# Optimization experiments

Measured on AMD Instinct MI355X. Metric: run time of the kernel, lower is better.

Reference implementation:

```python
import jax, jax.numpy as jnp
import numpy as np

N = 100000      # nodes
F_IN = 256      # num_node_features
E = 1600000     # edges (before self-loops)
DIMS = [F_IN, 128, 100, 32, 2]  # GCNConv layer widths


def _glorot(key, fan_in, fan_out):
    s = jnp.sqrt(6.0 / (fan_in + fan_out))
    return jax.random.uniform(key, (fan_in, fan_out), jnp.float32, -s, s)


def setup_inputs() -> dict:
    key = jax.random.key(0)
    ks = jax.random.split(key, 10)
    x = jax.random.normal(ks[0], (N, F_IN), jnp.float32)
    edge_index = jax.random.randint(ks[1], (2, E), 0, N, jnp.int32)
    inp = {"x": x, "edge_index": edge_index}
    for i in range(4):
        inp[f"W{i+1}"] = _glorot(ks[2 + 2 * i], DIMS[i], DIMS[i + 1])
        inp[f"b{i+1}"] = jnp.zeros((DIMS[i + 1],), jnp.float32)
    return inp


def reference(x, edge_index, W1, b1, W2, b2, W3, b3, W4, b4):
    n = x.shape[0]
    loops = jnp.arange(n, dtype=edge_index.dtype)
    src = jnp.concatenate([edge_index[0], loops])  # [E+N]
    dst = jnp.concatenate([edge_index[1], loops])
    # symmetric normalization: deg^-1/2[src] * deg^-1/2[dst] (self-loops included)
    deg = jax.ops.segment_sum(jnp.ones_like(src, x.dtype), dst, num_segments=n)
    dis = jax.lax.rsqrt(jnp.maximum(deg, 1.0))
    norm = (dis[src] * dis[dst])[:, None]  # [E+N, 1]

    def conv(h, W, b):
        h = h @ W                                      # [N, out]
        msg = h[src] * norm                            # gather + scale [E+N, out]
        return jax.ops.segment_sum(msg, dst, num_segments=n) + b

    h = jax.nn.leaky_relu(conv(x, W1, b1), negative_slope=0.1)
    h = jax.nn.leaky_relu(conv(h, W2, b2), negative_slope=0.1)
    h = jax.nn.leaky_relu(conv(h, W3, b3), negative_slope=0.1)
    h = conv(h, W4, b4)
    return jax.nn.softmax(h, axis=-1)
```

## Files before the change

### kernel.cpp

```cpp
#include <hip/hip_runtime.h>
#include <math.h>


typedef unsigned short ushort_t;
typedef unsigned int   uint_t;
typedef short  bf16x8 __attribute__((ext_vector_type(8)));
typedef float  f32x4  __attribute__((ext_vector_type(4)));

#define BKT_SHIFT 8
#define BKT_CAP   5120
#define BIN_CHUNK 4096

__device__ __forceinline__ ushort_t f2bf(float f) {
    union { float f; uint_t u; } v; v.f = f;
    uint_t u = v.u;
    u += 0x7fffu + ((u >> 16) & 1u);
    return (ushort_t)(u >> 16);
}
__device__ __forceinline__ float bflo(uint_t u) {
    union { uint_t q; float f; } v; v.q = u << 16; return v.f;
}
__device__ __forceinline__ float bfhi(uint_t u) {
    union { uint_t q; float f; } v; v.q = u & 0xffff0000u; return v.f;
}


__global__ __launch_bounds__(256) void bin_kernel(const int* __restrict__ srcArr,
                                                  const int* __restrict__ dstArr,
                                                  int* __restrict__ bkt_cursor,
                                                  uint2* __restrict__ staging,
                                                  int E, int nb) {
    __shared__ int hist[512];
    __shared__ int base[512];
    for (int b = threadIdx.x; b < 512; b += 256) hist[b] = 0;
    __syncthreads();
    const int e0 = blockIdx.x * BIN_CHUNK;
    #pragma unroll 4
    for (int k = 0; k < BIN_CHUNK / 256; ++k) {
        int e = e0 + k * 256 + threadIdx.x;
        if (e < E) atomicAdd(&hist[dstArr[e] >> BKT_SHIFT], 1);
    }
    __syncthreads();
    for (int b = threadIdx.x; b < nb; b += 256) {
        int h = hist[b];
        base[b] = h ? atomicAdd(&bkt_cursor[b], h) : 0;
    }
    __syncthreads();
    for (int b = threadIdx.x; b < 512; b += 256) hist[b] = 0;
    __syncthreads();
    #pragma unroll 4
    for (int k = 0; k < BIN_CHUNK / 256; ++k) {
        int e = e0 + k * 256 + threadIdx.x;
        if (e < E) {
            int s = srcArr[e], d = dstArr[e];
            int b = d >> BKT_SHIFT;
            int p = atomicAdd(&hist[b], 1);
            int idx = base[b] + p;
            if (idx < BKT_CAP)
                staging[(size_t)b * BKT_CAP + idx] = make_uint2((uint_t)s, (uint_t)d);
        }
    }
}

__global__ __launch_bounds__(512) void bucket_scan_kernel(const int* __restrict__ bkt_cursor,
                                                          int* __restrict__ bkt_base,
                                                          int* __restrict__ row_start,
                                                          int nbkt, int n) {
    __shared__ int buf[512];
    int v = ((int)threadIdx.x < nbkt) ? min(bkt_cursor[threadIdx.x], BKT_CAP) : 0;
    buf[threadIdx.x] = v;
    __syncthreads();
    for (int off = 1; off < 512; off <<= 1) {
        int t = (threadIdx.x >= (unsigned)off) ? buf[threadIdx.x - off] : 0;
        __syncthreads();
        buf[threadIdx.x] += t;
        __syncthreads();
    }
    if ((int)threadIdx.x < nbkt) bkt_base[threadIdx.x] = buf[threadIdx.x] - v;
    if ((int)threadIdx.x == nbkt - 1) row_start[n] = buf[threadIdx.x];
}

__global__ __launch_bounds__(256) void csr_build2_kernel(const uint2* __restrict__ staging,
                                                         const int* __restrict__ bkt_cursor,
                                                         const int* __restrict__ bkt_base,
                                                         int* __restrict__ row_start,
                                                         float* __restrict__ dis,
                                                         int* __restrict__ csr_src, int n) {
    __shared__ int cnt[256];
    __shared__ int buf[256];
    __shared__ int rsS[256];
    __shared__ int seg[BKT_CAP];
    const int t  = threadIdx.x;
    const int b  = blockIdx.x;
    const int lo = b << BKT_SHIFT;
    const int nl = min(256, n - lo);
    cnt[t] = 0;
    __syncthreads();
    const int cntE = min(bkt_cursor[b], BKT_CAP);
    for (int e = t; e < cntE; e += 256) {
        uint2 p = staging[(size_t)b * BKT_CAP + e];
        atomicAdd(&cnt[(int)p.y - lo], 1);
    }
    __syncthreads();
    const int v = cnt[t];
    buf[t] = v;
    __syncthreads();
    for (int off = 1; off < 256; off <<= 1) {
        int tt = (t >= off) ? buf[t - off] : 0;
        __syncthreads();
        buf[t] += tt;
        __syncthreads();
    }
    rsS[t] = buf[t] - v;
    const int sbase = bkt_base[b];
    if (t < nl) {
        row_start[lo + t] = sbase + (buf[t] - v);
        dis[lo + t] = rsqrtf((float)(v + 1));
    }
    cnt[t] = 0;
    __syncthreads();
    for (int e = t; e < cntE; e += 256) {
        uint2 p = staging[(size_t)b * BKT_CAP + e];
        int ln = (int)p.y - lo;
        int q  = atomicAdd(&cnt[ln], 1);
        seg[rsS[ln] + q] = (int)p.x;
    }
    __syncthreads();
    for (int i = t; i < cntE; i += 256) csr_src[sbase + i] = seg[i];
}


__global__ void cast_bf16_kernel(const float* __restrict__ in, ushort_t* __restrict__ out, int n8) {
    int i = blockIdx.x * blockDim.x + threadIdx.x;
    if (i >= n8) return;
    const float4 f0 = ((const float4*)in)[2 * i];
    const float4 f1 = ((const float4*)in)[2 * i + 1];
    uint4 o;
    o.x = (uint_t)f2bf(f0.x) | ((uint_t)f2bf(f0.y) << 16);
    o.y = (uint_t)f2bf(f0.z) | ((uint_t)f2bf(f0.w) << 16);
    o.z = (uint_t)f2bf(f1.x) | ((uint_t)f2bf(f1.y) << 16);
    o.w = (uint_t)f2bf(f1.z) | ((uint_t)f2bf(f1.w) << 16);
    ((uint4*)out)[i] = o;
}

__global__ void wt_all_kernel(const float* __restrict__ W1, const float* __restrict__ W2,
                              const float* __restrict__ W3,
                              ushort_t* __restrict__ Wt1, ushort_t* __restrict__ Wt2,
                              ushort_t* __restrict__ Wt3) {
    int idx = blockIdx.x * blockDim.x + threadIdx.x;
    if (idx < 32768) {
        int nn = idx >> 8, k = idx & 255;
        Wt1[idx] = f2bf(W1[(size_t)k * 128 + nn]);
    } else if (idx < 49152) {
        int j = idx - 32768;
        int nn = j >> 7, k = j & 127;
        float v = (nn < 100) ? W2[(size_t)k * 100 + nn] : 0.f;
        Wt2[j] = f2bf(v);
    } else if (idx < 57344) {
        int j = idx - 49152;
        int nn = j >> 7, k = j & 127;
        float v = (k < 100 && nn < 32) ? W3[(size_t)k * 32 + nn] : 0.f;
        Wt3[j] = f2bf(v);
    }
}

template <int NFR>
__global__ __launch_bounds__(256) void gemm_tile(const ushort_t* __restrict__ A,
                                                 const ushort_t* __restrict__ Bt,
                                                 ushort_t* __restrict__ C,
                                                 const float* __restrict__ dis,
                                                 int M, int K, int lda, int ldb, int ldc) {
    constexpr int BN = NFR * 32;
    __shared__ __attribute__((aligned(16))) ushort_t As[64][72];
    __shared__ __attribute__((aligned(16))) ushort_t Bs[BN][72];

    const int t    = threadIdx.x;
    const int lane = t & 63;
    const int w    = t >> 6;
    const int wm   = w >> 1, wn = w & 1;
    const int m0   = blockIdx.x * 64;
    const int rsel = lane & 15;
    const int q    = lane >> 4;

    f32x4 acc[2][NFR];
    #pragma unroll
    for (int mi = 0; mi < 2; ++mi)
        #pragma unroll
        for (int ni = 0; ni < NFR; ++ni) acc[mi][ni] = (f32x4){0.f, 0.f, 0.f, 0.f};

    const int srow = t >> 3;
    const int scol = (t & 7) * 8;

    for (int k0 = 0; k0 < K; k0 += 64) {
        #pragma unroll
        for (int it = 0; it < 2; ++it) {
            int r = srow + it * 32;
            int gm = m0 + r;
            bf16x8 v = {0, 0, 0, 0, 0, 0, 0, 0};
            if (gm < M) v = *(const bf16x8*)(A + (size_t)gm * lda + k0 + scol);
            *(bf16x8*)&As[r][scol] = v;
        }
        #pragma unroll
        for (int it = 0; it < BN / 32; ++it) {
            int r = srow + it * 32;
            bf16x8 v = *(const bf16x8*)(Bt + (size_t)r * ldb + k0 + scol);
            *(bf16x8*)&Bs[r][scol] = v;
        }
        __syncthreads();
        #pragma unroll
        for (int ks = 0; ks < 2; ++ks) {
            const int kc = ks * 32 + q * 8;
            bf16x8 af[2], bfr[NFR];
            #pragma unroll
            for (int mi = 0; mi < 2; ++mi)
                af[mi] = *(const bf16x8*)&As[wm * 32 + mi * 16 + rsel][kc];
            #pragma unroll
            for (int ni = 0; ni < NFR; ++ni)
                bfr[ni] = *(const bf16x8*)&Bs[wn * (BN / 2) + ni * 16 + rsel][kc];
            #pragma unroll
            for (int mi = 0; mi < 2; ++mi)
                #pragma unroll
                for (int ni = 0; ni < NFR; ++ni)
                    acc[mi][ni] = __builtin_amdgcn_mfma_f32_16x16x32_bf16(
                        bfr[ni], af[mi], acc[mi][ni], 0, 0, 0);
        }
        __syncthreads();
    }

    #pragma unroll
    for (int mi = 0; mi < 2; ++mi) {
        const int gm = m0 + wm * 32 + mi * 16 + rsel;
        if (gm >= M) continue;
        const float d = dis[gm];
        #pragma unroll
        for (int ni = 0; ni < NFR; ++ni) {
            uint2 o;
            o.x = (uint_t)f2bf(acc[mi][ni][0] * d) | ((uint_t)f2bf(acc[mi][ni][1] * d) << 16);
            o.y = (uint_t)f2bf(acc[mi][ni][2] * d) | ((uint_t)f2bf(acc[mi][ni][3] * d) << 16);
            *(uint2*)(C + (size_t)gm * ldc + wn * (BN / 2) + ni * 16 + q * 4) = o;
        }
    }
}

template <int F>
__global__ void aggregate128_kernel(const ushort_t* __restrict__ h, const int* __restrict__ row_start,
                                    const int* __restrict__ csr_src,
                                    const float* __restrict__ dis, const float* __restrict__ bias,
                                    ushort_t* __restrict__ out, int n) {
    int wid  = threadIdx.x >> 6;
    int lane = threadIdx.x & 63;
    int node = blockIdx.x * 4 + wid;
    if (node >= n) return;
    const int q    = lane >> 4;
    const uint_t fbb = (uint_t)(lane & 15) << 4;
    const char* hb = (const char*)h;
    float a[8];
    #pragma unroll
    for (int j = 0; j < 8; ++j) a[j] = 0.f;

    int i = row_start[node], end = row_start[node + 1];

#define LOADR(S) (*(const uint4*)(hb + (((uint_t)(S) << 8) + fbb)))
#define ACC8(U)                                                     \
    do {                                                            \
        a[0] += bflo((U).x); a[1] += bfhi((U).x);                   \
        a[2] += bflo((U).y); a[3] += bfhi((U).y);                   \
        a[4] += bflo((U).z); a[5] += bfhi((U).z);                   \
        a[6] += bflo((U).w); a[7] += bfhi((U).w);                   \
    } while (0)

    #pragma unroll 2
    for (; i + 8 <= end; i += 8) {
        int sA = csr_src[i + q];
        int sB = csr_src[i + 4 + q];
        uint4 u = LOADR(sA);
        uint4 v = LOADR(sB);
        ACC8(u);
        ACC8(v);
    }
    int r = end - i;
    if (r > 0) {
        if (q < r) {
            uint4 u = LOADR(csr_src[i + q]);
            ACC8(u);
        }
        if (q + 4 < r) {
            uint4 v = LOADR(csr_src[i + 4 + q]);
            ACC8(v);
        }
    }

    #pragma unroll
    for (int j = 0; j < 8; ++j) {
        a[j] += __shfl_xor(a[j], 16);
        a[j] += __shfl_xor(a[j], 32);
    }

    if (q == 0) {
        uint4 su = LOADR(node);
        ACC8(su);
        float dn = dis[node];
        const int fb = (lane & 15) * 8;
        #pragma unroll
        for (int j = 0; j < 8; ++j) {
            float b = (fb + j < F) ? bias[fb + j] : 0.f;
            float v = a[j] * dn + b;
            v = (v > 0.f) ? v : 0.1f * v;
            if (fb + j >= F) v = 0.f;
            a[j] = v;
        }
        uint4 o;
        o.x = (uint_t)f2bf(a[0]) | ((uint_t)f2bf(a[1]) << 16);
        o.y = (uint_t)f2bf(a[2]) | ((uint_t)f2bf(a[3]) << 16);
        o.z = (uint_t)f2bf(a[4]) | ((uint_t)f2bf(a[5]) << 16);
        o.w = (uint_t)f2bf(a[6]) | ((uint_t)f2bf(a[7]) << 16);
        *(uint4*)((char*)out + (((uint_t)node << 8) + fbb)) = o;
    }
#undef ACC8
#undef LOADR
}

__global__ void aggregate32_kernel(const ushort_t* __restrict__ h, const int* __restrict__ row_start,
                                   const int* __restrict__ csr_src,
                                   const float* __restrict__ dis, const float* __restrict__ bias,
                                   ushort_t* __restrict__ out, int n) {
    int lane16 = threadIdx.x & 15;
    int node = blockIdx.x * (blockDim.x >> 4) + (threadIdx.x >> 4);
    if (node >= n) return;
    const uint_t fbb = (uint_t)lane16 << 2;
    const char* hb = (const char*)h;
#define LOADR32(S) (*(const uint_t*)(hb + (((uint_t)(S) << 6) + fbb)))
    uint_t v = LOADR32(node);
    float acc0 = bflo(v);
    float acc1 = bfhi(v);
    int i = row_start[node], end = row_start[node + 1];
    for (; i + 4 <= end; i += 4) {
        uint_t u0 = LOADR32(csr_src[i]);
        uint_t u1 = LOADR32(csr_src[i + 1]);
        uint_t u2 = LOADR32(csr_src[i + 2]);
        uint_t u3 = LOADR32(csr_src[i + 3]);
        acc0 += bflo(u0) + bflo(u1) + bflo(u2) + bflo(u3);
        acc1 += bfhi(u0) + bfhi(u1) + bfhi(u2) + bfhi(u3);
    }
    for (; i < end; ++i) {
        uint_t u = LOADR32(csr_src[i]);
        acc0 += bflo(u); acc1 += bfhi(u);
    }
#undef LOADR32
    float dn = dis[node];
    const int f0 = 2 * lane16;
    acc0 = acc0 * dn + bias[f0];
    acc1 = acc1 * dn + bias[f0 + 1];
    acc0 = (acc0 > 0.f) ? acc0 : 0.1f * acc0;
    acc1 = (acc1 > 0.f) ? acc1 : 0.1f * acc1;
    uint_t o = (uint_t)f2bf(acc0) | ((uint_t)f2bf(acc1) << 16);
    *(uint_t*)((char*)out + (((uint_t)node << 6) + fbb)) = o;
}

__global__ void gemm32x2_kernel(const ushort_t* __restrict__ H, const float* __restrict__ W4,
                                const float* __restrict__ dis, float* __restrict__ C, int n) {
    int node = blockIdx.x * blockDim.x + threadIdx.x;
    if (node >= n) return;
    const uint_t* row = (const uint_t*)(H + (size_t)node * 32);
    float a0 = 0.f, a1 = 0.f;
    #pragma unroll
    for (int k2 = 0; k2 < 16; ++k2) {
        uint_t u = row[k2];
        float x0 = bflo(u), x1 = bfhi(u);
        int k = 2 * k2;
        a0 += x0 * W4[k * 2]     + x1 * W4[(k + 1) * 2];
        a1 += x0 * W4[k * 2 + 1] + x1 * W4[(k + 1) * 2 + 1];
    }
    float d = dis[node];
    C[2 * (size_t)node]     = a0 * d;
    C[2 * (size_t)node + 1] = a1 * d;
}

__global__ void aggregate2_softmax_kernel(const float* __restrict__ h, const int* __restrict__ row_start,
                                          const int* __restrict__ csr_src,
                                          const float* __restrict__ dis, const float* __restrict__ bias,
                                          float* __restrict__ out, int n) {
    int node = blockIdx.x * blockDim.x + threadIdx.x;
    if (node >= n) return;
    const char* hb = (const char*)h;
    float a0 = h[2 * (size_t)node];
    float a1 = h[2 * (size_t)node + 1];
    int beg = row_start[node], end = row_start[node + 1];
    for (int i = beg; i < end; ++i) {
        uint_t off = (uint_t)csr_src[i] << 3;
        float2 u = *(const float2*)(hb + off);
        a0 += u.x;
        a1 += u.y;
    }
    float dn = dis[node];
    a0 = a0 * dn + bias[0];
    a1 = a1 * dn + bias[1];
    float m  = fmaxf(a0, a1);
    float e0 = expf(a0 - m), e1 = expf(a1 - m);
    float inv = 1.f / (e0 + e1);
    out[2 * (size_t)node]     = e0 * inv;
    out[2 * (size_t)node + 1] = e1 * inv;
}


extern "C" void kernel_launch(void* const* d_in, const int* in_sizes, int n_in,
                              void* d_out, int out_size, void* d_ws, size_t ws_size,
                              hipStream_t stream) {
    const float* x  = (const float*)d_in[0];
    const int*   ei = (const int*)d_in[1];
    const float* W1 = (const float*)d_in[2];
    const float* b1 = (const float*)d_in[3];
    const float* W2 = (const float*)d_in[4];
    const float* b2 = (const float*)d_in[5];
    const float* W3 = (const float*)d_in[6];
    const float* b3 = (const float*)d_in[7];
    const float* W4 = (const float*)d_in[8];
    const float* b4 = (const float*)d_in[9];

    const int N = in_sizes[0] / 256;
    const int E = in_sizes[1] / 2;
    const int* srcA = ei;
    const int* dstA = ei + E;
    const int nbkt = (N + 255) >> BKT_SHIFT;

    char* ws = (char*)d_ws;
    size_t off = 0;
    auto alloc = [&](size_t bytes) {
        void* p = ws + off;
        off = (off + bytes + 255) & ~(size_t)255;
        return p;
    };
    float*    dis        = (float*)alloc((size_t)N * 4);
    int*      row_start  = (int*)alloc((size_t)(N + 1) * 4);
    int*      bkt_cursor = (int*)alloc(512 * 4);
    int*      bkt_base   = (int*)alloc(512 * 4);
    int*      csr_src    = (int*)alloc((size_t)E * 4);
    uint2*    staging    = (uint2*)alloc((size_t)nbkt * BKT_CAP * 8);
    ushort_t* xb         = (ushort_t*)alloc((size_t)N * 256 * 2);
    ushort_t* bufA       = (ushort_t*)alloc((size_t)N * 128 * 2);
    ushort_t* bufB       = (ushort_t*)alloc((size_t)N * 128 * 2);
    float*    C4         = (float*)alloc((size_t)N * 2 * 4);
    ushort_t* Wt1        = (ushort_t*)alloc((size_t)128 * 256 * 2);
    ushort_t* Wt2        = (ushort_t*)alloc((size_t)128 * 128 * 2);
    ushort_t* Wt3        = (ushort_t*)alloc((size_t)64 * 128 * 2);
    (void)ws_size;

    hipMemsetAsync(bkt_cursor, 0, 512 * 4, stream);

    bin_kernel<<<(E + BIN_CHUNK - 1) / BIN_CHUNK, 256, 0, stream>>>(
        srcA, dstA, bkt_cursor, staging, E, nbkt);
    bucket_scan_kernel<<<1, 512, 0, stream>>>(bkt_cursor, bkt_base, row_start, nbkt, N);
    csr_build2_kernel<<<nbkt, 256, 0, stream>>>(staging, bkt_cursor, bkt_base,
                                                row_start, dis, csr_src, N);

    wt_all_kernel<<<(57344 + 255) / 256, 256, 0, stream>>>(W1, W2, W3, Wt1, Wt2, Wt3);
    const int n8 = N * 32;
    cast_bf16_kernel<<<(n8 + 255) / 256, 256, 0, stream>>>(x, xb, n8);

    const int gx = (N + 63) / 64;
    const int aggBlocks128 = (N + 3) / 4;
    const int aggBlocks32  = (N + 15) / 16;

    gemm_tile<4><<<gx, 256, 0, stream>>>(xb, Wt1, bufA, dis, N, 256, 256, 256, 128);
    aggregate128_kernel<128><<<aggBlocks128, 256, 0, stream>>>(
        bufA, row_start, csr_src, dis, b1, bufB, N);
    gemm_tile<4><<<gx, 256, 0, stream>>>(bufB, Wt2, bufA, dis, N, 128, 128, 128, 128);
    aggregate128_kernel<100><<<aggBlocks128, 256, 0, stream>>>(
        bufA, row_start, csr_src, dis, b2, bufB, N);
    gemm_tile<1><<<gx, 256, 0, stream>>>(bufB, Wt3, bufA, dis, N, 128, 128, 128, 32);
    aggregate32_kernel<<<aggBlocks32, 256, 0, stream>>>(
        bufA, row_start, csr_src, dis, b3, bufB, N);
    gemm32x2_kernel<<<(N + 255) / 256, 256, 0, stream>>>(bufB, W4, dis, C4, N);
    aggregate2_softmax_kernel<<<(N + 255) / 256, 256, 0, stream>>>(
        C4, row_start, csr_src, dis, b4, (float*)d_out, N);
}
```

Before: 299.9 us.

## Map one node per 16-lane group in 128-wide aggregation instead of per wavefront

The 128-feature aggregation kernel now gives each 16-lane group its own destination node, so a wavefront handles four nodes at once instead of splitting one node's edges across four lane groups. This drops the cross-group shuffle reduction and the idle lanes in the epilogue, and the grid shrinks to match. In exchange, lanes within a wavefront now diverge on differing degrees and each group walks its edge list serially with a 4-way unrolled gather, which may lower memory-level parallelism per node.

Measured after the change: 299.3 us. No clear change (-0.2%).

```diff
diff --git a/kernel.cpp b/kernel.cpp
--- a/kernel.cpp
+++ b/kernel.cpp
@@ -247,18 +247,18 @@
                                     const int* __restrict__ csr_src,
                                     const float* __restrict__ dis, const float* __restrict__ bias,
                                     ushort_t* __restrict__ out, int n) {
-    int wid  = threadIdx.x >> 6;
-    int lane = threadIdx.x & 63;
-    int node = blockIdx.x * 4 + wid;
+    const int lane = threadIdx.x & 63;
+    const int grp  = lane >> 4;
+    const int node = blockIdx.x * 16 + (int)(threadIdx.x >> 6) * 4 + grp;
     if (node >= n) return;
-    const int q    = lane >> 4;
     const uint_t fbb = (uint_t)(lane & 15) << 4;
     const char* hb = (const char*)h;
     float a[8];
     #pragma unroll
     for (int j = 0; j < 8; ++j) a[j] = 0.f;
 
-    int i = row_start[node], end = row_start[node + 1];
+    int i = row_start[node];
+    const int end = row_start[node + 1];
 
 #define LOADR(S) (*(const uint4*)(hb + (((uint_t)(S) << 8) + fbb)))
 #define ACC8(U)                                                     \
@@ -269,53 +269,41 @@
         a[6] += bflo((U).w); a[7] += bfhi((U).w);                   \
     } while (0)
 
-    #pragma unroll 2
-    for (; i + 8 <= end; i += 8) {
-        int sA = csr_src[i + q];
-        int sB = csr_src[i + 4 + q];
-        uint4 u = LOADR(sA);
-        uint4 v = LOADR(sB);
+    for (; i + 4 <= end; i += 4) {
+        int s0 = csr_src[i];
+        int s1 = csr_src[i + 1];
+        int s2 = csr_src[i + 2];
+        int s3 = csr_src[i + 3];
+        uint4 u0 = LOADR(s0);
+        uint4 u1 = LOADR(s1);
+        uint4 u2 = LOADR(s2);
+        uint4 u3 = LOADR(s3);
+        ACC8(u0); ACC8(u1); ACC8(u2); ACC8(u3);
+    }
+    for (; i < end; ++i) {
+        uint4 u = LOADR(csr_src[i]);
         ACC8(u);
-        ACC8(v);
-    }
-    int r = end - i;
-    if (r > 0) {
-        if (q < r) {
-            uint4 u = LOADR(csr_src[i + q]);
-            ACC8(u);
-        }
-        if (q + 4 < r) {
-            uint4 v = LOADR(csr_src[i + 4 + q]);
-            ACC8(v);
-        }
-    }
-
+    }
+    {
+        uint4 su = LOADR(node);
+        ACC8(su);
+    }
+    float dn = dis[node];
+    const int fb = (lane & 15) * 8;
     #pragma unroll
     for (int j = 0; j < 8; ++j) {
-        a[j] += __shfl_xor(a[j], 16);
-        a[j] += __shfl_xor(a[j], 32);
-    }
-
-    if (q == 0) {
-        uint4 su = LOADR(node);
-        ACC8(su);
-        float dn = dis[node];
-        const int fb = (lane & 15) * 8;
-        #pragma unroll
-        for (int j = 0; j < 8; ++j) {
-            float b = (fb + j < F) ? bias[fb + j] : 0.f;
-            float v = a[j] * dn + b;
-            v = (v > 0.f) ? v : 0.1f * v;
-            if (fb + j >= F) v = 0.f;
-            a[j] = v;
-        }
-        uint4 o;
-        o.x = (uint_t)f2bf(a[0]) | ((uint_t)f2bf(a[1]) << 16);
-        o.y = (uint_t)f2bf(a[2]) | ((uint_t)f2bf(a[3]) << 16);
-        o.z = (uint_t)f2bf(a[4]) | ((uint_t)f2bf(a[5]) << 16);
-        o.w = (uint_t)f2bf(a[6]) | ((uint_t)f2bf(a[7]) << 16);
-        *(uint4*)((char*)out + (((uint_t)node << 8) + fbb)) = o;
-    }
+        float b = (fb + j < F) ? bias[fb + j] : 0.f;
+        float v = a[j] * dn + b;
+        v = (v > 0.f) ? v : 0.1f * v;
+        if (fb + j >= F) v = 0.f;
+        a[j] = v;
+    }
+    uint4 o;
+    o.x = (uint_t)f2bf(a[0]) | ((uint_t)f2bf(a[1]) << 16);
+    o.y = (uint_t)f2bf(a[2]) | ((uint_t)f2bf(a[3]) << 16);
+    o.z = (uint_t)f2bf(a[4]) | ((uint_t)f2bf(a[5]) << 16);
+    o.w = (uint_t)f2bf(a[6]) | ((uint_t)f2bf(a[7]) << 16);
+    *(uint4*)((char*)out + (((uint_t)node << 8) + fbb)) = o;
 #undef ACC8
 #undef LOADR
 }
@@ -458,7 +446,7 @@
     cast_bf16_kernel<<<(n8 + 255) / 256, 256, 0, stream>>>(x, xb, n8);
 
     const int gx = (N + 63) / 64;
-    const int aggBlocks128 = (N + 3) / 4;
+    const int aggBlocks128 = (N + 15) / 16;
     const int aggBlocks32  = (N + 15) / 16;
 
     gemm_tile<4><<<gx, 256, 0, stream>>>(xb, Wt1, bufA, dis, N, 256, 256, 256, 128);
```
